# Optimization experiments

Measured on AMD Instinct MI355X. Metric: run time of the kernel, lower is better.

Reference implementation:

```python
import jax, jax.numpy as jnp
import numpy as np

# Eigenvalue spec: (alpha, omega, multiplicity); field='complex' => d_state = sum(mul)
EIGS = [(-0.4, 0.0, 32), (-0.3, 3.14, 32), (-0.2, 6.28, 32), (-0.1, 12.57, 32),
        (-0.05, 25.13, 32), (-0.02, 50.27, 32), (-0.01, 100.53, 32), (-0.005, 201.06, 32)]
DELTA_MIN, DELTA_MAX = 1e-3, 1e-1
B_SZ, H, L = 8, 128, 8192  # batch, d_input, seq length


def setup_inputs() -> dict:
    key = jax.random.key(0)
    k_delta, k_bre, k_bim, k_cre, k_cim, k_d, k_u = jax.random.split(key, 7)
    # continuous-time diagonal state matrix Lambda (P,) complex
    Lam = np.concatenate([np.full(m, a + 1j * w, dtype=np.complex64) for a, w, m in EIGS])
    Lambda = jnp.asarray(Lam)  # (P,)
    P = Lambda.shape[0]
    # ZOH discretization (done at init in the torch module)
    Delta = DELTA_MIN + (DELTA_MAX - DELTA_MIN) * jax.random.uniform(k_delta, (P,), dtype=jnp.float32)
    Lambda_bar = jnp.exp(Lambda * Delta)  # (P,) complex64
    B = (jax.random.normal(k_bre, (P, H), dtype=jnp.float32)
         + 1j * jax.random.normal(k_bim, (P, H), dtype=jnp.float32))
    B_bar = (((Lambda_bar - 1.0) / Lambda)[:, None] * B).astype(jnp.complex64)  # (P,H)
    C_re = jax.random.normal(k_cre, (H, P), dtype=jnp.float32)
    C_im = jax.random.normal(k_cim, (H, P), dtype=jnp.float32)
    D = jax.random.normal(k_d, (H, H), dtype=jnp.float32)
    u = jax.random.normal(k_u, (B_SZ, H, L), dtype=jnp.float32)
    return {
        "u": u,
        "Lambda_bar_re": jnp.real(Lambda_bar), "Lambda_bar_im": jnp.imag(Lambda_bar),
        "B_bar_re": jnp.real(B_bar), "B_bar_im": jnp.imag(B_bar),
        "C_re": C_re, "C_im": C_im, "D": D,
    }


def reference(u, Lambda_bar_re, Lambda_bar_im, B_bar_re, B_bar_im, C_re, C_im, D):
    Lambda_bar = Lambda_bar_re + 1j * Lambda_bar_im          # (P,)
    B_bar = B_bar_re + 1j * B_bar_im                         # (P,H)
    C = C_re + 1j * C_im                                     # (H,P)
    uc = u.astype(B_bar.dtype)
    Bu = jnp.einsum('ph,bhl->bpl', B_bar, uc)                # (B,P,L) complex
    A = jnp.broadcast_to(Lambda_bar[None, :, None], Bu.shape)  # (B,P,L)
    # The repo's binary op computes the sequential recurrence x_t = A_t * (x_{t-1} + Bu_t).
    # Rewriting with Bu'_t = A_t * Bu_t gives x_t = A_t x_{t-1} + Bu'_t, which is the
    # standard (truly associative) first-order scan.
    ABu = A * Bu

    def binop(ei, ej):
        a_i, b_i = ei
        a_j, b_j = ej
        return a_j * a_i, a_j * b_i + b_j

    _, xs = jax.lax.associative_scan(binop, (A, ABu), axis=2)  # xs: (B,P,L)
    y = jnp.einsum('op,bpl->bol', C, xs).real + jnp.einsum('oh,bhl->bol', D, u)
    return jax.nn.gelu(y, approximate=False)  # torch nn.GELU default = exact erf
```

## Files before the change

kernel.cpp:

```cpp
#include <hip/hip_runtime.h>
#include <math.h>

#define Bn 8
#define Hd 128
#define Ld 8192
#define Pd 256
#define LC 32
#define NC 256

typedef __attribute__((ext_vector_type(8))) short bf16x8;
typedef __attribute__((ext_vector_type(4))) float f32x4;
#define MFMA16(a, b, c) __builtin_amdgcn_mfma_f32_16x16x32_bf16(a, b, c, 0, 0, 0)

__device__ __forceinline__ unsigned short f2bf(float f) {
  unsigned u = __float_as_uint(f);
  u = u + 0x7fffu + ((u >> 16) & 1u);
  return (unsigned short)(u >> 16);
}

#if __has_builtin(__builtin_amdgcn_cvt_pk_bf16_f32)
typedef __attribute__((ext_vector_type(2))) __bf16 v2bf_t;
__device__ __forceinline__ unsigned pack2(float a, float b) {
  v2bf_t r = __builtin_amdgcn_cvt_pk_bf16_f32(a, b);
  unsigned u;
  __builtin_memcpy(&u, &r, 4);
  return u;
}
#else
__device__ __forceinline__ unsigned pack2(float a, float b) {
  return (unsigned)f2bf(a) | ((unsigned)f2bf(b) << 16);
}
#endif

__device__ __forceinline__ float bflo(unsigned v) { return __uint_as_float(v << 16); }
__device__ __forceinline__ float bfhi(unsigned v) { return __uint_as_float(v & 0xffff0000u); }

__device__ __forceinline__ int bperm(int p) {
  return ((p & 4) << 2) | ((p & 16) >> 1) | ((p & 8) >> 1) | (p & 3);
}

__global__ void k_prep(const float* __restrict__ Bre, const float* __restrict__ Bim,
                       const float* __restrict__ Cre, const float* __restrict__ Cim,
                       const float* __restrict__ Dm,
                       bf16x8* __restrict__ Bfr, bf16x8* __restrict__ Bfi,
                       bf16x8* __restrict__ Cf, bf16x8* __restrict__ Df) {
  int tid = blockIdx.x * 256 + threadIdx.x;
  int lane = tid & 63, slot = tid >> 6;
  int q = lane >> 4, ln = lane & 15;
  if (slot < 64) {
    int ks = slot >> 4, mt = slot & 15;
    int p = mt * 16 + ln;
    bf16x8 vr, vi;
#pragma unroll
    for (int e = 0; e < 8; ++e) {
      int h = ks * 32 + q * 8 + e;
      vr[e] = (short)f2bf(Bre[p * Hd + h]);
      vi[e] = (short)f2bf(Bim[p * Hd + h]);
    }
    Bfr[slot * 64 + lane] = vr;
    Bfi[slot * 64 + lane] = vi;
  } else if (slot < 64 + 128) {
    int s2 = slot - 64;
    int ks = s2 >> 3, mt = s2 & 7;
    int o = mt * 16 + ln;
    bf16x8 v;
#pragma unroll
    for (int e = 0; e < 8; ++e) {
      int kp = ks * 32 + q * 8 + e;
      int p = kp >> 1;
      float val = (kp & 1) ? -Cim[o * Pd + p] : Cre[o * Pd + p];
      v[e] = (short)f2bf(val);
    }
    Cf[s2 * 64 + lane] = v;
  } else if (slot < 64 + 128 + 32) {
    int s3 = slot - 192;
    int ks = s3 >> 3, mt = s3 & 7;
    int o = mt * 16 + ln;
    bf16x8 v;
#pragma unroll
    for (int e = 0; e < 8; ++e) {
      int h = ks * 32 + q * 8 + e;
      v[e] = (short)f2bf(Dm[o * Hd + h]);
    }
    Df[s3 * 64 + lane] = v;
  }
}

__device__ __forceinline__ void stage_u(const float* __restrict__ ub, unsigned* us32, int t) {
  int lane = t & 63, w = t >> 6;
  int j0 = 4 * (lane & 7);
  int h2 = 16 * w + 2 * (lane >> 3);
  const float* r0 = ub + (size_t)h2 * Ld + j0;
  float4 a0 = *(const float4*)r0;
  float4 a1 = *(const float4*)(r0 + Ld);
  const float* r2 = r0 + (size_t)64 * Ld;
  float4 b0 = *(const float4*)r2;
  float4 b1 = *(const float4*)(r2 + Ld);
  float ta0[4] = {a0.x, a0.y, a0.z, a0.w};
  float ta1[4] = {a1.x, a1.y, a1.z, a1.w};
  float tb0[4] = {b0.x, b0.y, b0.z, b0.w};
  float tb1[4] = {b1.x, b1.y, b1.z, b1.w};
#pragma unroll
  for (int i = 0; i < 4; ++i) {
    int j = j0 + i;
    int g1 = (h2 >> 3) ^ (j & 7);
    us32[(j * 256 + (g1 << 4) + ((2 * h2) & 15)) >> 2] = pack2(ta0[i], ta1[i]);
    int hb = h2 + 64;
    int g2 = (hb >> 3) ^ (j & 7);
    us32[(j * 256 + (g2 << 4) + ((2 * hb) & 15)) >> 2] = pack2(tb0[i], tb1[i]);
  }
}

__device__ __forceinline__ void compute_bu(const unsigned* us32,
                                           const bf16x8* __restrict__ Bfr,
                                           const bf16x8* __restrict__ Bfi,
                                           unsigned* bu32, int t) {
  int lane = t & 63, w = t >> 6, q = lane >> 4, ln = lane & 15;
  f32x4 zz = {0.f, 0.f, 0.f, 0.f};
  f32x4 aR[4][2], aI[4][2];
#pragma unroll
  for (int mt = 0; mt < 4; ++mt)
#pragma unroll
    for (int n = 0; n < 2; ++n) { aR[mt][n] = zz; aI[mt][n] = zz; }

#pragma unroll
  for (int ks = 0; ks < 4; ++ks) {
    bf16x8 ubf[2];
#pragma unroll
    for (int n = 0; n < 2; ++n) {
      int j = 16 * n + ln;
      int g = (4 * ks + q) ^ (j & 7);
      ubf[n] = *(const bf16x8*)((const char*)us32 + j * 256 + g * 16);
    }
#pragma unroll
    for (int mt = 0; mt < 4; ++mt) {
      int tI = ks * 16 + w * 4 + mt;
      bf16x8 ar = Bfr[tI * 64 + lane];
      bf16x8 ai = Bfi[tI * 64 + lane];
#pragma unroll
      for (int n = 0; n < 2; ++n) {
        aR[mt][n] = MFMA16(ar, ubf[n], aR[mt][n]);
        aI[mt][n] = MFMA16(ai, ubf[n], aI[mt][n]);
      }
    }
  }
#pragma unroll
  for (int mt = 0; mt < 4; ++mt)
#pragma unroll
    for (int n = 0; n < 2; ++n)
#pragma unroll
      for (int r = 0; r < 4; ++r) {
        int p = w * 64 + mt * 16 + q * 4 + r;
        int j = 16 * n + ln;
        bu32[(p << 5) | (j ^ bperm(p))] = pack2(aR[mt][n][r], aI[mt][n][r]);
      }
}

__global__ __launch_bounds__(256, 4) void k_chunk(
    const float* __restrict__ u, const float* __restrict__ lre,
    const float* __restrict__ lim, const bf16x8* __restrict__ Bfr,
    const bf16x8* __restrict__ Bfi, float2* __restrict__ E) {
  int bc = blockIdx.x;
  int b = bc >> 8, c = bc & 255;
  __shared__ __align__(16) unsigned char smem[8192 + 32768];
  unsigned* us32 = (unsigned*)smem;
  unsigned* bu32 = (unsigned*)(smem + 8192);
  int t = threadIdx.x;

  stage_u(u + (size_t)b * Hd * Ld + c * LC, us32, t);
  __syncthreads();
  compute_bu(us32, Bfr, Bfi, bu32, t);
  __syncthreads();

  int p = t;
  int pm = bperm(p);
  float ax = lre[p], ay = lim[p];
  float xr = 0.f, xi = 0.f;
#pragma unroll
  for (int j = 0; j < LC; ++j) {
    unsigned v = bu32[(p << 5) | (j ^ pm)];
    float sr = xr + bflo(v), si = xi + bfhi(v);
    xr = ax * sr - ay * si;
    xi = ax * si + ay * sr;
  }
  E[(size_t)bc * Pd + p] = make_float2(xr, xi);
}

__global__ __launch_bounds__(256) void k_scan(const float* __restrict__ lre,
                                              const float* __restrict__ lim,
                                              float2* __restrict__ E) {
  int g = blockIdx.x * 256 + threadIdx.x;
  int b = g >> 11;
  int p = (g >> 3) & 255;
  int rq = g & 7;
  float ax = lre[p], ay = lim[p];
  float sx = ax, sy = ay;
#pragma unroll
  for (int k = 0; k < 5; ++k) {
    float nx = sx * sx - sy * sy, ny = 2.f * sx * sy;
    sx = nx; sy = ny;
  }
  size_t base = ((size_t)(b * NC + rq * 32)) * Pd + p;
  float2 pre[32];
  float cr = 0.f, ci = 0.f;
#pragma unroll 8
  for (int i = 0; i < 32; ++i) {
    float2 e = E[base + (size_t)i * Pd];
    pre[i] = make_float2(cr, ci);
    float nx = sx * cr - sy * ci + e.x;
    float ny = sx * ci + sy * cr + e.y;
    cr = nx; ci = ny;
  }
  float Sx = sx, Sy = sy;
#pragma unroll
  for (int k = 0; k < 5; ++k) {
    float nx = Sx * Sx - Sy * Sy, ny = 2.f * Sx * Sy;
    Sx = nx; Sy = ny;
  }
  float Vx = cr, Vy = ci;
  float Mx = Sx, My = Sy;
#pragma unroll
  for (int d = 1; d < 8; d <<= 1) {
    float ux = __shfl_up(Vx, d, 8);
    float uy = __shfl_up(Vy, d, 8);
    if (rq >= d) {
      Vx += Mx * ux - My * uy;
      Vy += Mx * uy + My * ux;
    }
    float nx = Mx * Mx - My * My, ny = 2.f * Mx * My;
    Mx = nx; My = ny;
  }
  float Cx = __shfl_up(Vx, 1, 8);
  float Cy = __shfl_up(Vy, 1, 8);
  if (rq == 0) { Cx = 0.f; Cy = 0.f; }
  float tx = 1.f, ty = 0.f;
#pragma unroll 8
  for (int i = 0; i < 32; ++i) {
    float ox = pre[i].x + tx * Cx - ty * Cy;
    float oy = pre[i].y + tx * Cy + ty * Cx;
    E[base + (size_t)i * Pd] = make_float2(ox, oy);
    float nx = tx * sx - ty * sy, ny = tx * sy + ty * sx;
    tx = nx; ty = ny;
  }
}

__global__ __launch_bounds__(256, 4) void k_main(
    const float* __restrict__ u, const float* __restrict__ lre,
    const float* __restrict__ lim, const bf16x8* __restrict__ Bfr,
    const bf16x8* __restrict__ Bfi, const bf16x8* __restrict__ Cf,
    const bf16x8* __restrict__ Df, const float2* __restrict__ E,
    float* __restrict__ out) {
  int bc = blockIdx.x;
  int b = bc >> 8, c = bc & 255;
  __shared__ __align__(16) unsigned char smem[8192 + 32768];
  unsigned* us32 = (unsigned*)smem;
  unsigned* bu32 = (unsigned*)(smem + 8192);
  unsigned* xs32 = bu32;
  int t = threadIdx.x;
  int lane = t & 63, w = t >> 6, q = lane >> 4, ln = lane & 15;

  stage_u(u + (size_t)b * Hd * Ld + c * LC, us32, t);
  __syncthreads();
  compute_bu(us32, Bfr, Bfi, bu32, t);
  __syncthreads();

  int p = t;
  int pm = bperm(p);
  unsigned v[LC];
#pragma unroll
  for (int j = 0; j < LC; ++j) v[j] = bu32[(p << 5) | (j ^ pm)];
  float2 xin = E[(size_t)bc * Pd + p];
  __syncthreads();

  {
    float ax = lre[p], ay = lim[p];
    float xr = xin.x, xi = xin.y;
#pragma unroll
    for (int j = 0; j < LC; ++j) {
      float sr = xr + bflo(v[j]), si = xi + bfhi(v[j]);
      xr = ax * sr - ay * si;
      xi = ax * si + ay * sr;
      xs32[j * 256 + ((((p >> 2) ^ (j & 7)) << 2) + (p & 3))] = pack2(xr, xi);
    }
  }
  __syncthreads();

  f32x4 zz = {0.f, 0.f, 0.f, 0.f};
  f32x4 acc[2][2] = {{zz, zz}, {zz, zz}};
#pragma unroll
  for (int ks = 0; ks < 16; ++ks) {
    bf16x8 xb[2];
#pragma unroll
    for (int n = 0; n < 2; ++n) {
      int j = 16 * n + ln;
      int g = (4 * ks + q) ^ (j & 7);
      xb[n] = *(const bf16x8*)((const char*)xs32 + j * 1024 + g * 16);
    }
#pragma unroll
    for (int mt = 0; mt < 2; ++mt) {
      bf16x8 cf = Cf[(ks * 8 + w * 2 + mt) * 64 + lane];
#pragma unroll
      for (int n = 0; n < 2; ++n) acc[mt][n] = MFMA16(cf, xb[n], acc[mt][n]);
    }
  }
#pragma unroll
  for (int ks = 0; ks < 4; ++ks) {
    bf16x8 ubf[2];
#pragma unroll
    for (int n = 0; n < 2; ++n) {
      int j = 16 * n + ln;
      int g = (4 * ks + q) ^ (j & 7);
      ubf[n] = *(const bf16x8*)((const char*)us32 + j * 256 + g * 16);
    }
#pragma unroll
    for (int mt = 0; mt < 2; ++mt) {
      bf16x8 df = Df[(ks * 8 + w * 2 + mt) * 64 + lane];
#pragma unroll
      for (int n = 0; n < 2; ++n) acc[mt][n] = MFMA16(df, ubf[n], acc[mt][n]);
    }
  }

#pragma unroll
  for (int mt = 0; mt < 2; ++mt)
#pragma unroll
    for (int n = 0; n < 2; ++n)
#pragma unroll
      for (int r = 0; r < 4; ++r) {
        int o = w * 32 + mt * 16 + q * 4 + r;
        int l = c * LC + 16 * n + ln;
        float vy = acc[mt][n][r];
        float e2 = __builtin_amdgcn_exp2f(-2.4554670f * vy);
        float gy = vy * __builtin_amdgcn_rcpf(1.0f + e2);
        out[((size_t)(b * Hd + o)) * Ld + l] = gy;
      }
}

extern "C" void kernel_launch(void* const* d_in, const int* in_sizes, int n_in,
                              void* d_out, int out_size, void* d_ws, size_t ws_size,
                              hipStream_t stream) {
  const float* u   = (const float*)d_in[0];
  const float* lre = (const float*)d_in[1];
  const float* lim = (const float*)d_in[2];
  const float* Bre = (const float*)d_in[3];
  const float* Bim = (const float*)d_in[4];
  const float* Cre = (const float*)d_in[5];
  const float* Cim = (const float*)d_in[6];
  const float* Dm  = (const float*)d_in[7];
  float* out = (float*)d_out;

  char* ws = (char*)d_ws;
  bf16x8* Bfr = (bf16x8*)(ws);
  bf16x8* Bfi = (bf16x8*)(ws + 65536);
  bf16x8* Cf  = (bf16x8*)(ws + 131072);
  bf16x8* Df  = (bf16x8*)(ws + 262144);
  float2* E   = (float2*)(ws + (1 << 20));

  k_prep<<<56, 256, 0, stream>>>(Bre, Bim, Cre, Cim, Dm, Bfr, Bfi, Cf, Df);
  k_chunk<<<Bn * NC, 256, 0, stream>>>(u, lre, lim, Bfr, Bfi, E);
  k_scan<<<64, 256, 0, stream>>>(lre, lim, E);
  k_main<<<Bn * NC, 256, 0, stream>>>(u, lre, lim, Bfr, Bfi, Cf, Df, E, out);
}
```

Baseline: 154.4 us.

## Cache Bu projection in global memory and widen chunk-scan parallelism

k_chunk stores its computed bf16 Bu tile per chunk to a global workspace so k_main can load it instead of recomputing the B-projection MFMA. The inter-chunk scan kernel is restructured to use more blocks, with a shared-memory Hillis-Steele scan over 32 segments of 8 chunks. This trades recompute for a large extra global write and read of the Bu tensor and needs additional workspace.

```diff
diff --git a/kernel.cpp b/kernel.cpp
--- a/kernel.cpp
+++ b/kernel.cpp
@@ -159,7 +159,8 @@
 __global__ __launch_bounds__(256, 4) void k_chunk(
     const float* __restrict__ u, const float* __restrict__ lre,
     const float* __restrict__ lim, const bf16x8* __restrict__ Bfr,
-    const bf16x8* __restrict__ Bfi, float2* __restrict__ E) {
+    const bf16x8* __restrict__ Bfi, float2* __restrict__ E,
+    uint4* __restrict__ bu_g) {
   int bc = blockIdx.x;
   int b = bc >> 8, c = bc & 255;
   __shared__ __align__(16) unsigned char smem[8192 + 32768];
@@ -174,113 +175,126 @@
 
   int p = t;
   int pm = bperm(p);
+  unsigned v[LC];
+#pragma unroll
+  for (int j = 0; j < LC; ++j) v[j] = bu32[(p << 5) | (j ^ pm)];
+
   float ax = lre[p], ay = lim[p];
   float xr = 0.f, xi = 0.f;
 #pragma unroll
   for (int j = 0; j < LC; ++j) {
-    unsigned v = bu32[(p << 5) | (j ^ pm)];
-    float sr = xr + bflo(v), si = xi + bfhi(v);
+    float sr = xr + bflo(v[j]), si = xi + bfhi(v[j]);
     xr = ax * sr - ay * si;
     xi = ax * si + ay * sr;
   }
   E[(size_t)bc * Pd + p] = make_float2(xr, xi);
+  uint4* dst = bu_g + ((size_t)bc * Pd + p) * 8;
+#pragma unroll
+  for (int i = 0; i < 8; ++i)
+    dst[i] = make_uint4(v[4 * i + 0], v[4 * i + 1], v[4 * i + 2], v[4 * i + 3]);
 }
 
 __global__ __launch_bounds__(256) void k_scan(const float* __restrict__ lre,
                                               const float* __restrict__ lim,
                                               float2* __restrict__ E) {
-  int g = blockIdx.x * 256 + threadIdx.x;
-  int b = g >> 11;
-  int p = (g >> 3) & 255;
-  int rq = g & 7;
+  __shared__ float2 arr[32][8];
+  int nb = blockIdx.x;
+  int t = threadIdx.x;
+  int pl = t & 7, rq = t >> 3;
+  int b = nb >> 5;
+  int p = ((nb & 31) << 3) + pl;
   float ax = lre[p], ay = lim[p];
-  float sx = ax, sy = ay;
+  float mx = ax, my = ay;
 #pragma unroll
   for (int k = 0; k < 5; ++k) {
-    float nx = sx * sx - sy * sy, ny = 2.f * sx * sy;
-    sx = nx; sy = ny;
-  }
-  size_t base = ((size_t)(b * NC + rq * 32)) * Pd + p;
-  float2 pre[32];
+    float nx = mx * mx - my * my, ny = 2.f * mx * my;
+    mx = nx; my = ny;
+  }
+  size_t base = ((size_t)(b * NC + rq * 8)) * Pd + p;
+  float2 pre[8];
   float cr = 0.f, ci = 0.f;
-#pragma unroll 8
-  for (int i = 0; i < 32; ++i) {
+#pragma unroll
+  for (int i = 0; i < 8; ++i) {
     float2 e = E[base + (size_t)i * Pd];
     pre[i] = make_float2(cr, ci);
-    float nx = sx * cr - sy * ci + e.x;
-    float ny = sx * ci + sy * cr + e.y;
+    float nx = mx * cr - my * ci + e.x;
+    float ny = mx * ci + my * cr + e.y;
     cr = nx; ci = ny;
   }
-  float Sx = sx, Sy = sy;
-#pragma unroll
-  for (int k = 0; k < 5; ++k) {
-    float nx = Sx * Sx - Sy * Sy, ny = 2.f * Sx * Sy;
-    Sx = nx; Sy = ny;
-  }
-  float Vx = cr, Vy = ci;
-  float Mx = Sx, My = Sy;
-#pragma unroll
-  for (int d = 1; d < 8; d <<= 1) {
-    float ux = __shfl_up(Vx, d, 8);
-    float uy = __shfl_up(Vy, d, 8);
-    if (rq >= d) {
-      Vx += Mx * ux - My * uy;
-      Vy += Mx * uy + My * ux;
-    }
+  float Mx = mx, My = my;
+#pragma unroll
+  for (int k = 0; k < 3; ++k) {
     float nx = Mx * Mx - My * My, ny = 2.f * Mx * My;
     Mx = nx; My = ny;
   }
-  float Cx = __shfl_up(Vx, 1, 8);
-  float Cy = __shfl_up(Vy, 1, 8);
-  if (rq == 0) { Cx = 0.f; Cy = 0.f; }
+  float Vx = cr, Vy = ci;
+#pragma unroll
+  for (int d = 1; d < 32; d <<= 1) {
+    arr[rq][pl] = make_float2(Vx, Vy);
+    __syncthreads();
+    if (rq >= d) {
+      float2 pv = arr[rq - d][pl];
+      Vx += Mx * pv.x - My * pv.y;
+      Vy += Mx * pv.y + My * pv.x;
+    }
+    __syncthreads();
+    float nx = Mx * Mx - My * My, ny = 2.f * Mx * My;
+    Mx = nx; My = ny;
+  }
+  arr[rq][pl] = make_float2(Vx, Vy);
+  __syncthreads();
+  float Cx = 0.f, Cy = 0.f;
+  if (rq > 0) {
+    float2 pv = arr[rq - 1][pl];
+    Cx = pv.x; Cy = pv.y;
+  }
   float tx = 1.f, ty = 0.f;
-#pragma unroll 8
-  for (int i = 0; i < 32; ++i) {
+#pragma unroll
+  for (int i = 0; i < 8; ++i) {
     float ox = pre[i].x + tx * Cx - ty * Cy;
     float oy = pre[i].y + tx * Cy + ty * Cx;
     E[base + (size_t)i * Pd] = make_float2(ox, oy);
-    float nx = tx * sx - ty * sy, ny = tx * sy + ty * sx;
+    float nx = tx * mx - ty * my, ny = tx * my + ty * mx;
     tx = nx; ty = ny;
   }
 }
 
 __global__ __launch_bounds__(256, 4) void k_main(
     const float* __restrict__ u, const float* __restrict__ lre,
-    const float* __restrict__ lim, const bf16x8* __restrict__ Bfr,
-    const bf16x8* __restrict__ Bfi, const bf16x8* __restrict__ Cf,
+    const float* __restrict__ lim, const bf16x8* __restrict__ Cf,
     const bf16x8* __restrict__ Df, const float2* __restrict__ E,
-    float* __restrict__ out) {
+    const uint4* __restrict__ bu_g, float* __restrict__ out) {
   int bc = blockIdx.x;
   int b = bc >> 8, c = bc & 255;
   __shared__ __align__(16) unsigned char smem[8192 + 32768];
   unsigned* us32 = (unsigned*)smem;
-  unsigned* bu32 = (unsigned*)(smem + 8192);
-  unsigned* xs32 = bu32;
+  unsigned* xs32 = (unsigned*)(smem + 8192);
   int t = threadIdx.x;
   int lane = t & 63, w = t >> 6, q = lane >> 4, ln = lane & 15;
 
   stage_u(u + (size_t)b * Hd * Ld + c * LC, us32, t);
-  __syncthreads();
-  compute_bu(us32, Bfr, Bfi, bu32, t);
-  __syncthreads();
 
   int p = t;
-  int pm = bperm(p);
-  unsigned v[LC];
-#pragma unroll
-  for (int j = 0; j < LC; ++j) v[j] = bu32[(p << 5) | (j ^ pm)];
+  const uint4* src = bu_g + ((size_t)bc * Pd + p) * 8;
+  uint4 bv[8];
+#pragma unroll
+  for (int i = 0; i < 8; ++i) bv[i] = src[i];
   float2 xin = E[(size_t)bc * Pd + p];
-  __syncthreads();
-
   {
     float ax = lre[p], ay = lim[p];
     float xr = xin.x, xi = xin.y;
 #pragma unroll
-    for (int j = 0; j < LC; ++j) {
-      float sr = xr + bflo(v[j]), si = xi + bfhi(v[j]);
-      xr = ax * sr - ay * si;
-      xi = ax * si + ay * sr;
-      xs32[j * 256 + ((((p >> 2) ^ (j & 7)) << 2) + (p & 3))] = pack2(xr, xi);
+    for (int i = 0; i < 8; ++i) {
+      unsigned ww[4] = {bv[i].x, bv[i].y, bv[i].z, bv[i].w};
+#pragma unroll
+      for (int e = 0; e < 4; ++e) {
+        int j = 4 * i + e;
+        unsigned vj = ww[e];
+        float sr = xr + bflo(vj), si = xi + bfhi(vj);
+        xr = ax * sr - ay * si;
+        xi = ax * si + ay * sr;
+        xs32[j * 256 + ((((p >> 2) ^ (j & 7)) << 2) + (p & 3))] = pack2(xr, xi);
+      }
     }
   }
   __syncthreads();
@@ -354,9 +368,10 @@
   bf16x8* Cf  = (bf16x8*)(ws + 131072);
   bf16x8* Df  = (bf16x8*)(ws + 262144);
   float2* E   = (float2*)(ws + (1 << 20));
+  uint4*  buw = (uint4*)(ws + (8u << 20));
 
   k_prep<<<56, 256, 0, stream>>>(Bre, Bim, Cre, Cim, Dm, Bfr, Bfi, Cf, Df);
-  k_chunk<<<Bn * NC, 256, 0, stream>>>(u, lre, lim, Bfr, Bfi, E);
-  k_scan<<<64, 256, 0, stream>>>(lre, lim, E);
-  k_main<<<Bn * NC, 256, 0, stream>>>(u, lre, lim, Bfr, Bfi, Cf, Df, E, out);
-}
+  k_chunk<<<Bn * NC, 256, 0, stream>>>(u, lre, lim, Bfr, Bfi, E, buw);
+  k_scan<<<256, 256, 0, stream>>>(lre, lim, E);
+  k_main<<<Bn * NC, 256, 0, stream>>>(u, lre, lim, Cf, Df, E, (const uint4*)buw, out);
+}
```

Result: slower. 163.3 us (+5.7%).
